# Kernel optimization log

Hardware: AMD Instinct MI355X
Metric: run time of the kernel (lower is better)

## Reference

```python
import jax, jax.numpy as jnp
import numpy as np

B, N = 65536, 32
Z = jnp.array([0.0, 0.0, 1.0], dtype=jnp.float32)  # joint rotation axis
G = 9.81  # gravity magnitude along +z of base frame (matches base_lin_acc[:,2]=9.81)


def skew(v):
    # [..., 3] -> [..., 3, 3] skew-symmetric matrix
    x, y, z = v[..., 0], v[..., 1], v[..., 2]
    o = jnp.zeros_like(x)
    return jnp.stack([jnp.stack([o, -z, y], -1),
                      jnp.stack([z, o, -x], -1),
                      jnp.stack([-y, x, o], -1)], -2)


def rot_z(q):
    # [B] -> [B, 3, 3] rotation about z (revolute joint)
    c, s = jnp.cos(q), jnp.sin(q)
    o, l = jnp.zeros_like(q), jnp.ones_like(q)
    return jnp.stack([jnp.stack([c, -s, o], -1),
                      jnp.stack([s, c, o], -1),
                      jnp.stack([o, o, l], -1)], -2)


def setup_inputs() -> dict:
    key = jax.random.key(0)
    ks = jax.random.split(key, 8)
    return {
        "q": jax.random.normal(ks[0], (B, N), jnp.float32),
        "qd": jax.random.normal(ks[1], (B, N), jnp.float32),
        "qdd_des": jax.random.normal(ks[2], (B, N), jnp.float32),
        "trans": jax.random.uniform(ks[3], (N, 3), jnp.float32),      # fixed joint-origin offsets
        "mass": jax.random.uniform(ks[4], (N,), jnp.float32) + 0.1,   # positive link masses
        "com": jax.random.uniform(ks[5], (N, 3), jnp.float32),        # center of mass per link
        "inertia": jax.random.normal(ks[6], (N, 3, 3), jnp.float32),  # rotational inertia (about CoM)
        "damping": jax.random.uniform(ks[7], (N,), jnp.float32),      # joint damping consts
    }


def reference(q, qd, qdd_des, trans, mass, com, inertia, damping):
    """Recursive Newton-Euler inverse dynamics (compute_inverse_dynamics),
    for a serial chain of N revolute-z joints, include_gravity=True."""
    Bn = q.shape[0]
    mcom = mass[:, None] * com                                        # [N,3]
    S = skew(com)                                                     # [N,3,3]
    # spatial inertia: I + m * skew(c) @ skew(c)^T (multiply_motion_vec)
    Ibar = inertia + mass[:, None, None] * (S @ jnp.swapaxes(S, -1, -2))

    def fwd_step(carry, xs):
        # propagate velocity/acceleration from parent into child body frame
        v_lin, v_ang, a_lin, a_ang = carry
        qj, qdj, qddj, p = xs
        R = rot_z(qj)                                                 # joint_pose rotation [B,3,3]
        Rt = jnp.swapaxes(R, -1, -2)
        t = -jnp.einsum('bij,j->bi', Rt, p)                           # inverse() translation
        # SpatialMotionVec.transform: ang' = R ang ; lin' = t x ang' + R lin
        wv = jnp.einsum('bij,bj->bi', Rt, v_ang)
        lv = jnp.cross(t, wv) + jnp.einsum('bij,bj->bi', Rt, v_lin)
        wa = jnp.einsum('bij,bj->bi', Rt, a_ang)
        la = jnp.cross(t, wa) + jnp.einsum('bij,bj->bi', Rt, a_lin)
        jv = qdj[:, None] * Z                                         # joint_vel (ang only)
        ja = qddj[:, None] * Z                                        # joint_acc (ang only)
        v_ang_n = wv + jv
        v_lin_n = lv
        # acc = parent_acc + joint_acc + vel x joint_vel (cross_motion_vec)
        a_ang_n = wa + ja + jnp.cross(v_ang_n, jv)
        a_lin_n = la + jnp.cross(v_lin_n, jv)
        c = (v_lin_n, v_ang_n, a_lin_n, a_ang_n)
        return c, (v_lin_n, v_ang_n, a_lin_n, a_ang_n, R)

    zeros3 = jnp.zeros((Bn, 3), q.dtype)
    base_lin_acc = zeros3.at[:, 2].set(jnp.asarray(G, q.dtype))       # gravity as base acc
    init = (zeros3, zeros3, base_lin_acc, zeros3)
    xs = (q.T, qd.T, qdd_des.T, trans)
    _, (v_lin_s, v_ang_s, a_lin_s, a_ang_s, R_s) = jax.lax.scan(fwd_step, init, xs)

    def bwd_step(carry, xs):
        # backward force recursion: f_i = I a_i + v_i x* (I v_i) + X(joint_pose_{i+1}) f_{i+1}
        g_lin, g_ang = carry
        v_lin, v_ang, a_lin, a_ang, R, p, m, mc, Ib = xs
        # inertia.multiply_motion_vec on acc and vel
        fa_lin = m * a_lin + jnp.cross(mc[None, :], a_ang)
        fa_ang = jnp.einsum('ij,bj->bi', Ib, a_ang) + jnp.cross(mc[None, :], a_lin)
        fv_lin = m * v_lin + jnp.cross(mc[None, :], v_ang)
        fv_ang = jnp.einsum('ij,bj->bi', Ib, v_ang) + jnp.cross(mc[None, :], v_lin)
        # vel.cross_force_vec(I v)
        cf_ang = jnp.cross(v_ang, fv_ang) + jnp.cross(v_lin, fv_lin)
        cf_lin = jnp.cross(v_ang, fv_lin)
        f_lin = fa_lin + cf_lin + g_lin
        f_ang = fa_ang + cf_ang + g_ang
        tau = f_ang[:, 2]                                             # force.ang . z_axis
        # SpatialForceVec.transform by this body's joint_pose (into parent frame)
        Rf = jnp.einsum('bij,bj->bi', R, f_lin)
        out_ang = jnp.cross(p[None, :], Rf) + jnp.einsum('bij,bj->bi', R, f_ang)
        return (Rf, out_ang), tau

    xs_b = (v_lin_s, v_ang_s, a_lin_s, a_ang_s, R_s, trans, mass, mcom, Ibar)
    _, taus = jax.lax.scan(bwd_step, (zeros3, zeros3), xs_b, reverse=True)
    # taus: [N, B]; add joint damping term: damping * qd
    return taus.T + damping[None, :] * qd
```

## Files before the change

### kernel.cpp

```cpp
#include <hip/hip_runtime.h>

#define NJ 32
#define BLK 256

template<int CTRL, int ROW, int BANK>
__device__ __forceinline__ float dpp0(float x) {
    return __int_as_float(
        __builtin_amdgcn_update_dpp(0, __float_as_int(x), CTRL, ROW, BANK, false));
}

__device__ __forceinline__ float scan32(float x) {
    x += dpp0<0x111, 0xf, 0xf>(x);
    x += dpp0<0x112, 0xf, 0xf>(x);
    x += dpp0<0x114, 0xf, 0xe>(x);
    x += dpp0<0x118, 0xf, 0xc>(x);
    x += dpp0<0x142, 0xa, 0xf>(x);
    return x;
}

__device__ __forceinline__ float bcast31(float x) {
    return __int_as_float(
        __builtin_amdgcn_ds_swizzle(__float_as_int(x), 0x03E0));
}

__global__ __launch_bounds__(BLK) void rnea_kernel(
    const float* __restrict__ q,
    const float* __restrict__ qd,
    const float* __restrict__ qdd,
    const float* __restrict__ trans,
    const float* __restrict__ mass,
    const float* __restrict__ com,
    const float* __restrict__ inertia,
    const float* __restrict__ damping,
    float* __restrict__ out,
    int Bn)
{
    const int t    = blockIdx.x * BLK + threadIdx.x;
    const int lane = threadIdx.x & 31;
    const int row  = t >> 5;
    if (row >= Bn) return;
    const size_t idx = (size_t)row * NJ + lane;

    float qj   = q  [idx];
    float qdj  = qd [idx];
    float qddj = qdd[idx];

    float m    = mass[lane];
    float cx   = com[3*lane+0], cy = com[3*lane+1];
    float mcx  = m*cx, mcy = m*cy;
    float i2z  = fmaf(m, cx*cx + cy*cy, inertia[9*lane+8]);
    float px   = trans[3*lane+0], py = trans[3*lane+1];
    float damp = damping[lane];

    float phi = scan32(qj);
    float wI  = scan32(qdj);
    float aI  = scan32(qddj);
    float wP  = wI - qdj;
    float aP  = aI - qddj;

    float c, s, cp, sp;
    __sincosf(phi, &s, &c);
    __sincosf(phi - qj, &sp, &cp);

    float dx = cp*px - sp*py;
    float dy = sp*px + cp*py;

    float VLx = scan32(-wP*dy);
    float VLy = scan32( wP*dx);

    float ALx = scan32(fmaf(-aP, dy,  qdj*VLy));
    float ALy = scan32(fmaf( aP, dx, -qdj*VLx));

    float mcwx = c*mcx - s*mcy;
    float mcwy = s*mcx + c*mcy;

    float fv_lx = fmaf(m, VLx,  wI*mcwy);
    float fv_ly = fmaf(m, VLy, -wI*mcwx);

    float llx = fmaf(m, ALx, fmaf( aI, mcwy, -wI*fv_ly));
    float lly = fmaf(m, ALy, fmaf(-aI, mcwx,  wI*fv_lx));

    float Px = scan32(llx);
    float Py = scan32(lly);
    float Fx = bcast31(Px) - Px + llx;
    float Fy = bcast31(Py) - Py + lly;

    float a = fmaf(aI, i2z, mcwx*ALy - mcwy*ALx + VLx*fv_ly - VLy*fv_lx);
    float b = dx*Fy - dy*Fx;
    float ab = a + b;
    float Pr = scan32(ab);
    float Nz = bcast31(Pr) - Pr + ab - b;

    out[idx] = fmaf(damp, qdj, Nz);
}

extern "C" void kernel_launch(void* const* d_in, const int* in_sizes, int n_in,
                              void* d_out, int out_size, void* d_ws, size_t ws_size,
                              hipStream_t stream) {
    const float* q       = (const float*)d_in[0];
    const float* qd      = (const float*)d_in[1];
    const float* qdd     = (const float*)d_in[2];
    const float* trans   = (const float*)d_in[3];
    const float* mass    = (const float*)d_in[4];
    const float* com     = (const float*)d_in[5];
    const float* inertia = (const float*)d_in[6];
    const float* damping = (const float*)d_in[7];
    float* out = (float*)d_out;

    int Bn = in_sizes[0] / NJ;
    long long threads = (long long)Bn * 32;
    int grid = (int)((threads + BLK - 1) / BLK);
    hipLaunchKernelGGL(rnea_kernel, dim3(grid), dim3(BLK), 0, stream,
                       q, qd, qdd, trans, mass, com, inertia, damping, out, Bn);
}
```

Measured before the change: 15.52 us.

## Process two batch rows per thread and replace second sincos with DPP lane shift

Each thread now handles two rows, half a batch apart, which halves the grid and amortizes the per-lane constant loads across both rows. The parent-frame cos/sin is taken from the neighbouring lane with a DPP row shift instead of a second sincos call, with lane 0 forced to the identity. Launch bounds gain an occupancy hint. The risks are higher register pressure and less parallelism; an odd batch size would leave the last row unprocessed, and the wave_shr1 shift control must carry values across 16-lane row boundaries for the result to stay correct.

```diff
diff --git a/kernel.cpp b/kernel.cpp
--- a/kernel.cpp
+++ b/kernel.cpp
@@ -18,12 +18,69 @@
     return x;
 }
 
+__device__ __forceinline__ float wave_shr1(float x) {
+    return __int_as_float(
+        __builtin_amdgcn_update_dpp(0, __float_as_int(x), 0x138, 0xf, 0xf, false));
+}
+
 __device__ __forceinline__ float bcast31(float x) {
     return __int_as_float(
         __builtin_amdgcn_ds_swizzle(__float_as_int(x), 0x03E0));
 }
 
-__global__ __launch_bounds__(BLK) void rnea_kernel(
+struct Consts {
+    float m, mcx, mcy, i2z, px, py, damp;
+};
+
+__device__ __forceinline__ float tau_row(float qj, float qdj, float qddj,
+                                         bool seg0, const Consts& C)
+{
+    float phi = scan32(qj);
+    float wI  = scan32(qdj);
+    float aI  = scan32(qddj);
+    float wP  = wI - qdj;
+    float aP  = aI - qddj;
+
+    float c, s;
+    __sincosf(phi, &s, &c);
+    float cp = wave_shr1(c);
+    float sp = wave_shr1(s);
+    cp = seg0 ? 1.f : cp;
+    sp = seg0 ? 0.f : sp;
+
+    float dx = cp*C.px - sp*C.py;
+    float dy = sp*C.px + cp*C.py;
+
+    float VLx = scan32(-wP*dy);
+    float VLy = scan32( wP*dx);
+
+    float ALx = scan32(fmaf(-aP, dy,  qdj*VLy));
+    float ALy = scan32(fmaf( aP, dx, -qdj*VLx));
+
+    float mcwx = c*C.mcx - s*C.mcy;
+    float mcwy = s*C.mcx + c*C.mcy;
+
+    float fv_lx = fmaf(C.m, VLx,  wI*mcwy);
+    float fv_ly = fmaf(C.m, VLy, -wI*mcwx);
+
+    float llx = fmaf(C.m, ALx, fmaf( aI, mcwy, -wI*fv_ly));
+    float lly = fmaf(C.m, ALy, fmaf(-aI, mcwx,  wI*fv_lx));
+
+    float Px = scan32(llx);
+    float Py = scan32(lly);
+    float Fx = bcast31(Px) - Px + llx;
+    float Fy = bcast31(Py) - Py + lly;
+
+    float a = fmaf(aI, C.i2z, mcwx*ALy - mcwy*ALx + VLx*fv_ly - VLy*fv_lx);
+    float b = dx*Fy - dy*Fx;
+    float ab = a + b;
+    float Pr = scan32(ab);
+    float Nz = bcast31(Pr) - Pr + ab - b;
+
+    return fmaf(C.damp, qdj, Nz);
+}
+
+__global__ __launch_bounds__(BLK, 4) void rnea_kernel(
     const float* __restrict__ q,
     const float* __restrict__ qd,
     const float* __restrict__ qdd,
@@ -37,61 +94,32 @@
 {
     const int t    = blockIdx.x * BLK + threadIdx.x;
     const int lane = threadIdx.x & 31;
-    const int row  = t >> 5;
-    if (row >= Bn) return;
-    const size_t idx = (size_t)row * NJ + lane;
+    const int half = Bn >> 1;
+    const int r0   = t >> 5;
+    if (r0 >= half) return;
+    const size_t i0 = (size_t)r0 * NJ + lane;
+    const size_t i1 = i0 + (size_t)half * NJ;
 
-    float qj   = q  [idx];
-    float qdj  = qd [idx];
-    float qddj = qdd[idx];
+    float q0   = q  [i0], q1   = q  [i1];
+    float qd0  = qd [i0], qd1  = qd [i1];
+    float qdd0 = qdd[i0], qdd1 = qdd[i1];
 
-    float m    = mass[lane];
-    float cx   = com[3*lane+0], cy = com[3*lane+1];
-    float mcx  = m*cx, mcy = m*cy;
-    float i2z  = fmaf(m, cx*cx + cy*cy, inertia[9*lane+8]);
-    float px   = trans[3*lane+0], py = trans[3*lane+1];
-    float damp = damping[lane];
+    Consts C;
+    C.m    = mass[lane];
+    float cx = com[3*lane+0], cy = com[3*lane+1];
+    C.mcx  = C.m*cx;  C.mcy = C.m*cy;
+    C.i2z  = fmaf(C.m, cx*cx + cy*cy, inertia[9*lane+8]);
+    C.px   = trans[3*lane+0];
+    C.py   = trans[3*lane+1];
+    C.damp = damping[lane];
 
-    float phi = scan32(qj);
-    float wI  = scan32(qdj);
-    float aI  = scan32(qddj);
-    float wP  = wI - qdj;
-    float aP  = aI - qddj;
+    const bool seg0 = (lane == 0);
 
-    float c, s, cp, sp;
-    __sincosf(phi, &s, &c);
-    __sincosf(phi - qj, &sp, &cp);
+    float t0 = tau_row(q0, qd0, qdd0, seg0, C);
+    float t1 = tau_row(q1, qd1, qdd1, seg0, C);
 
-    float dx = cp*px - sp*py;
-    float dy = sp*px + cp*py;
-
-    float VLx = scan32(-wP*dy);
-    float VLy = scan32( wP*dx);
-
-    float ALx = scan32(fmaf(-aP, dy,  qdj*VLy));
-    float ALy = scan32(fmaf( aP, dx, -qdj*VLx));
-
-    float mcwx = c*mcx - s*mcy;
-    float mcwy = s*mcx + c*mcy;
-
-    float fv_lx = fmaf(m, VLx,  wI*mcwy);
-    float fv_ly = fmaf(m, VLy, -wI*mcwx);
-
-    float llx = fmaf(m, ALx, fmaf( aI, mcwy, -wI*fv_ly));
-    float lly = fmaf(m, ALy, fmaf(-aI, mcwx,  wI*fv_lx));
-
-    float Px = scan32(llx);
-    float Py = scan32(lly);
-    float Fx = bcast31(Px) - Px + llx;
-    float Fy = bcast31(Py) - Py + lly;
-
-    float a = fmaf(aI, i2z, mcwx*ALy - mcwy*ALx + VLx*fv_ly - VLy*fv_lx);
-    float b = dx*Fy - dy*Fx;
-    float ab = a + b;
-    float Pr = scan32(ab);
-    float Nz = bcast31(Pr) - Pr + ab - b;
-
-    out[idx] = fmaf(damp, qdj, Nz);
+    out[i0] = t0;
+    out[i1] = t1;
 }
 
 extern "C" void kernel_launch(void* const* d_in, const int* in_sizes, int n_in,
@@ -108,7 +136,7 @@
     float* out = (float*)d_out;
 
     int Bn = in_sizes[0] / NJ;
-    long long threads = (long long)Bn * 32;
+    long long threads = (long long)(Bn/2) * 32;
     int grid = (int)((threads + BLK - 1) / BLK);
     hipLaunchKernelGGL(rnea_kernel, dim3(grid), dim3(BLK), 0, stream,
                        q, qd, qdd, trans, mass, com, inertia, damping, out, Bn);
```

Measured after the change: 15.57 us. About the same (+0.3%).

## Process two batch rows per thread with batched inline-asm DPP scans

Applied to the files above, without the earlier changes.

Each thread now handles two batch rows (one from each half of the batch), so the DPP scan steps for six or four independent values are interleaved in hand-written inline assembly to hide DPP latency. The parent-frame sin/cos is taken from the neighbouring lane with a wave shift-right DPP instead of a second sincos, and the fast sincos uses the hardware sin/cos instructions on a fractional revolution. Segment totals come from readlane instead of ds_swizzle. This halves the thread count and raises per-thread ILP, at the cost of fragile inline asm that relies on manual s_nop hazard handling and on Bn being even.

```diff
diff --git a/kernel.cpp b/kernel.cpp
--- a/kernel.cpp
+++ b/kernel.cpp
@@ -3,24 +3,69 @@
 #define NJ 32
 #define BLK 256
 
-template<int CTRL, int ROW, int BANK>
-__device__ __forceinline__ float dpp0(float x) {
-    return __int_as_float(
-        __builtin_amdgcn_update_dpp(0, __float_as_int(x), CTRL, ROW, BANK, false));
+
+#define MODS1 "row_shr:1 row_mask:0xf bank_mask:0xf bound_ctrl:0"
+#define MODS2 "row_shr:2 row_mask:0xf bank_mask:0xf bound_ctrl:0"
+#define MODS4 "row_shr:4 row_mask:0xf bank_mask:0xf bound_ctrl:0"
+#define MODS8 "row_shr:8 row_mask:0xf bank_mask:0xf bound_ctrl:0"
+#define MODSB "row_bcast:15 row_mask:0xa bank_mask:0xf"
+
+#define STEP6(m) \
+  "v_add_f32_dpp %0, %0, %0 " m "\n\t" \
+  "v_add_f32_dpp %1, %1, %1 " m "\n\t" \
+  "v_add_f32_dpp %2, %2, %2 " m "\n\t" \
+  "v_add_f32_dpp %3, %3, %3 " m "\n\t" \
+  "v_add_f32_dpp %4, %4, %4 " m "\n\t" \
+  "v_add_f32_dpp %5, %5, %5 " m "\n\t"
+
+#define STEP4(m) \
+  "v_add_f32_dpp %0, %0, %0 " m "\n\t" \
+  "v_add_f32_dpp %1, %1, %1 " m "\n\t" \
+  "v_add_f32_dpp %2, %2, %2 " m "\n\t" \
+  "v_add_f32_dpp %3, %3, %3 " m "\n\t"
+
+#define STEP2(m) \
+  "v_add_f32_dpp %0, %0, %0 " m "\n\t" \
+  "v_add_f32_dpp %1, %1, %1 " m "\n\t" \
+  "s_nop 0\n\t"
+
+__device__ __forceinline__ void scan6(float& a, float& b, float& c,
+                                      float& d, float& e, float& f) {
+    asm("s_nop 1\n\t"
+        STEP6(MODS1) STEP6(MODS2) STEP6(MODS4) STEP6(MODS8) STEP6(MODSB)
+        : "+v"(a), "+v"(b), "+v"(c), "+v"(d), "+v"(e), "+v"(f));
 }
 
-__device__ __forceinline__ float scan32(float x) {
-    x += dpp0<0x111, 0xf, 0xf>(x);
-    x += dpp0<0x112, 0xf, 0xf>(x);
-    x += dpp0<0x114, 0xf, 0xe>(x);
-    x += dpp0<0x118, 0xf, 0xc>(x);
-    x += dpp0<0x142, 0xa, 0xf>(x);
-    return x;
+__device__ __forceinline__ void scan4(float& a, float& b, float& c, float& d) {
+    asm("s_nop 1\n\t"
+        STEP4(MODS1) STEP4(MODS2) STEP4(MODS4) STEP4(MODS8) STEP4(MODSB)
+        : "+v"(a), "+v"(b), "+v"(c), "+v"(d));
 }
 
-__device__ __forceinline__ float bcast31(float x) {
+__device__ __forceinline__ void scan2(float& a, float& b) {
+    asm("s_nop 1\n\t"
+        STEP2(MODS1) STEP2(MODS2) STEP2(MODS4) STEP2(MODS8) STEP2(MODSB)
+        : "+v"(a), "+v"(b));
+}
+
+__device__ __forceinline__ float seg_total(float x, int hiHalf) {
+    int lo, hi;
+    asm("s_nop 1\n\t"
+        "v_readlane_b32 %0, %2, 31\n\t"
+        "v_readlane_b32 %1, %2, 63"
+        : "=s"(lo), "=s"(hi) : "v"(x));
+    return __int_as_float(hiHalf ? hi : lo);
+}
+
+__device__ __forceinline__ float wave_shr1(float x) {
     return __int_as_float(
-        __builtin_amdgcn_ds_swizzle(__float_as_int(x), 0x03E0));
+        __builtin_amdgcn_update_dpp(0, __float_as_int(x), 0x138, 0xf, 0xf, false));
+}
+
+__device__ __forceinline__ void fast_sincos(float x, float& s, float& c) {
+    float r = __builtin_amdgcn_fractf(x * 0.15915494309189535f);
+    s = __builtin_amdgcn_sinf(r);
+    c = __builtin_amdgcn_cosf(r);
 }
 
 __global__ __launch_bounds__(BLK) void rnea_kernel(
@@ -37,13 +82,16 @@
 {
     const int t    = blockIdx.x * BLK + threadIdx.x;
     const int lane = threadIdx.x & 31;
-    const int row  = t >> 5;
-    if (row >= Bn) return;
-    const size_t idx = (size_t)row * NJ + lane;
+    const int hiH  = (threadIdx.x >> 5) & 1;
+    const int half = Bn >> 1;
+    const int r0   = t >> 5;
+    if (r0 >= half) return;
+    const size_t i0 = (size_t)r0 * NJ + lane;
+    const size_t i1 = i0 + (size_t)half * NJ;
 
-    float qj   = q  [idx];
-    float qdj  = qd [idx];
-    float qddj = qdd[idx];
+    float q0   = q  [i0], q1   = q  [i1];
+    float qd0  = qd [i0], qd1  = qd [i1];
+    float qdd0 = qdd[i0], qdd1 = qdd[i1];
 
     float m    = mass[lane];
     float cx   = com[3*lane+0], cy = com[3*lane+1];
@@ -51,47 +99,66 @@
     float i2z  = fmaf(m, cx*cx + cy*cy, inertia[9*lane+8]);
     float px   = trans[3*lane+0], py = trans[3*lane+1];
     float damp = damping[lane];
+    const bool seg0 = (lane == 0);
 
-    float phi = scan32(qj);
-    float wI  = scan32(qdj);
-    float aI  = scan32(qddj);
-    float wP  = wI - qdj;
-    float aP  = aI - qddj;
+    float phi0 = q0, phi1 = q1, wI0 = qd0, wI1 = qd1, aI0 = qdd0, aI1 = qdd1;
+    scan6(phi0, phi1, wI0, wI1, aI0, aI1);
+    float wP0 = wI0 - qd0,  wP1 = wI1 - qd1;
+    float aP0 = aI0 - qdd0, aP1 = aI1 - qdd1;
 
-    float c, s, cp, sp;
-    __sincosf(phi, &s, &c);
-    __sincosf(phi - qj, &sp, &cp);
+    float c0, s0, c1, s1;
+    fast_sincos(phi0, s0, c0);
+    fast_sincos(phi1, s1, c1);
+    float cp0 = wave_shr1(c0), sp0 = wave_shr1(s0);
+    float cp1 = wave_shr1(c1), sp1 = wave_shr1(s1);
+    cp0 = seg0 ? 1.f : cp0;  sp0 = seg0 ? 0.f : sp0;
+    cp1 = seg0 ? 1.f : cp1;  sp1 = seg0 ? 0.f : sp1;
 
-    float dx = cp*px - sp*py;
-    float dy = sp*px + cp*py;
+    float dx0 = cp0*px - sp0*py, dy0 = sp0*px + cp0*py;
+    float dx1 = cp1*px - sp1*py, dy1 = sp1*px + cp1*py;
 
-    float VLx = scan32(-wP*dy);
-    float VLy = scan32( wP*dx);
+    float VLx0 = -wP0*dy0, VLy0 = wP0*dx0;
+    float VLx1 = -wP1*dy1, VLy1 = wP1*dx1;
+    scan4(VLx0, VLy0, VLx1, VLy1);
 
-    float ALx = scan32(fmaf(-aP, dy,  qdj*VLy));
-    float ALy = scan32(fmaf( aP, dx, -qdj*VLx));
+    float ALx0 = fmaf(-aP0, dy0,  qd0*VLy0);
+    float ALy0 = fmaf( aP0, dx0, -qd0*VLx0);
+    float ALx1 = fmaf(-aP1, dy1,  qd1*VLy1);
+    float ALy1 = fmaf( aP1, dx1, -qd1*VLx1);
+    scan4(ALx0, ALy0, ALx1, ALy1);
 
-    float mcwx = c*mcx - s*mcy;
-    float mcwy = s*mcx + c*mcy;
+    float mcwx0 = c0*mcx - s0*mcy, mcwy0 = s0*mcx + c0*mcy;
+    float mcwx1 = c1*mcx - s1*mcy, mcwy1 = s1*mcx + c1*mcy;
 
-    float fv_lx = fmaf(m, VLx,  wI*mcwy);
-    float fv_ly = fmaf(m, VLy, -wI*mcwx);
+    float fv_lx0 = fmaf(m, VLx0,  wI0*mcwy0);
+    float fv_ly0 = fmaf(m, VLy0, -wI0*mcwx0);
+    float fv_lx1 = fmaf(m, VLx1,  wI1*mcwy1);
+    float fv_ly1 = fmaf(m, VLy1, -wI1*mcwx1);
 
-    float llx = fmaf(m, ALx, fmaf( aI, mcwy, -wI*fv_ly));
-    float lly = fmaf(m, ALy, fmaf(-aI, mcwx,  wI*fv_lx));
+    float llx0 = fmaf(m, ALx0, fmaf( aI0, mcwy0, -wI0*fv_ly0));
+    float lly0 = fmaf(m, ALy0, fmaf(-aI0, mcwx0,  wI0*fv_lx0));
+    float llx1 = fmaf(m, ALx1, fmaf( aI1, mcwy1, -wI1*fv_ly1));
+    float lly1 = fmaf(m, ALy1, fmaf(-aI1, mcwx1,  wI1*fv_lx1));
 
-    float Px = scan32(llx);
-    float Py = scan32(lly);
-    float Fx = bcast31(Px) - Px + llx;
-    float Fy = bcast31(Py) - Py + lly;
+    float Px0 = llx0, Py0 = lly0, Px1 = llx1, Py1 = lly1;
+    scan4(Px0, Py0, Px1, Py1);
+    float Fx0 = seg_total(Px0, hiH) - Px0 + llx0;
+    float Fy0 = seg_total(Py0, hiH) - Py0 + lly0;
+    float Fx1 = seg_total(Px1, hiH) - Px1 + llx1;
+    float Fy1 = seg_total(Py1, hiH) - Py1 + lly1;
 
-    float a = fmaf(aI, i2z, mcwx*ALy - mcwy*ALx + VLx*fv_ly - VLy*fv_lx);
-    float b = dx*Fy - dy*Fx;
-    float ab = a + b;
-    float Pr = scan32(ab);
-    float Nz = bcast31(Pr) - Pr + ab - b;
+    float a0 = fmaf(aI0, i2z, mcwx0*ALy0 - mcwy0*ALx0 + VLx0*fv_ly0 - VLy0*fv_lx0);
+    float a1 = fmaf(aI1, i2z, mcwx1*ALy1 - mcwy1*ALx1 + VLx1*fv_ly1 - VLy1*fv_lx1);
+    float b0 = dx0*Fy0 - dy0*Fx0;
+    float b1 = dx1*Fy1 - dy1*Fx1;
+    float ab0 = a0 + b0, ab1 = a1 + b1;
+    float Pr0 = ab0, Pr1 = ab1;
+    scan2(Pr0, Pr1);
+    float Nz0 = seg_total(Pr0, hiH) - Pr0 + ab0 - b0;
+    float Nz1 = seg_total(Pr1, hiH) - Pr1 + ab1 - b1;
 
-    out[idx] = fmaf(damp, qdj, Nz);
+    out[i0] = fmaf(damp, qd0, Nz0);
+    out[i1] = fmaf(damp, qd1, Nz1);
 }
 
 extern "C" void kernel_launch(void* const* d_in, const int* in_sizes, int n_in,
@@ -108,7 +175,7 @@
     float* out = (float*)d_out;
 
     int Bn = in_sizes[0] / NJ;
-    long long threads = (long long)Bn * 32;
+    long long threads = (long long)(Bn/2) * 32;
     int grid = (int)((threads + BLK - 1) / BLK);
     hipLaunchKernelGGL(rnea_kernel, dim3(grid), dim3(BLK), 0, stream,
                        q, qd, qdd, trans, mass, com, inertia, damping, out, Bn);
```

After: 14.19 us. 1.09x faster.
